# Performance work log

Hardware: AMD Instinct MI355X
Metric: run time of the kernel (lower is better)

The kernel has to match this reference:

```python
import jax, jax.numpy as jnp
import numpy as np

B = 1_048_576
W = 64  # hidden width
N_FREQ = 6   # 3 dims * 6 freqs * (sin,cos) = 36
K_BLOB = 4   # one-blob bins per dim


def _freq_embed(p):
    # [B,3] -> [B,36]
    freqs = 2.0 ** jnp.arange(N_FREQ, dtype=p.dtype)
    ang = jnp.pi * p[:, :, None] * freqs  # [B,3,6]
    return jnp.concatenate([jnp.sin(ang), jnp.cos(ang)], axis=-1).reshape(p.shape[0], 3 * 2 * N_FREQ)


def _sph(d):
    # unit-square parameterization of a direction, [B,3] -> [B,2]
    d = d / (jnp.linalg.norm(d, axis=-1, keepdims=True) + 1e-8)
    u = jnp.arctan2(d[:, 1], d[:, 0]) / (2.0 * jnp.pi) + 0.5
    v = jnp.arccos(jnp.clip(d[:, 2], -1.0 + 1e-6, 1.0 - 1e-6)) / jnp.pi
    return jnp.stack([u, v], axis=-1)


def _one_blob(x, k=K_BLOB):
    # x in [0,1], [B,D] -> [B,D*k] Gaussian one-blob encoding
    centers = (jnp.arange(k, dtype=x.dtype) + 0.5) / k
    sigma = 1.0 / k
    g = jnp.exp(-0.5 * ((x[..., None] - centers) / sigma) ** 2)  # [B,D,k]
    return g.reshape(x.shape[0], -1)


def _encode(p, wi, n, alpha, beta, r):
    ones = jnp.ones((p.shape[0], 2), dtype=p.dtype)
    return jnp.concatenate([
        _freq_embed(p),                      # 36
        _one_blob(_sph(wi)),                 # 8
        _one_blob(_sph(n)),                  # 8
        _one_blob(1.0 - jnp.exp(-r)),        # 4
        alpha, beta,                         # 6
        ones,                                # 2 (implicit bias)
    ], axis=-1)                              # -> [B,64]


def _mlp(x, Ws):
    h = x
    for Wk in Ws[:-1]:
        h = jax.nn.relu(h @ Wk.T)
    return h @ Ws[-1].T  # [B,3]


def setup_inputs() -> dict:
    key = jax.random.key(0)
    ks = jax.random.split(key, 13)
    p = jax.random.normal(ks[0], (B, 3), jnp.float32)
    wi = jax.random.normal(ks[1], (B, 3), jnp.float32)
    n = jax.random.normal(ks[2], (B, 3), jnp.float32)
    alpha = jax.random.uniform(ks[3], (B, 3), jnp.float32)
    beta = jax.random.uniform(ks[4], (B, 3), jnp.float32)
    r = jax.random.uniform(ks[5], (B, 1), jnp.float32)
    s = 1.0 / np.sqrt(W)
    weights = {}
    for i in range(6):
        weights[f"W{i}"] = jax.random.normal(ks[6 + i], (W, W), jnp.float32) * s
    weights["W6"] = jax.random.normal(ks[12], (3, W), jnp.float32) * s
    return dict(p=p, wi=wi, n=n, alpha=alpha, beta=beta, r=r, **weights)


def reference(p, wi, n, alpha, beta, r, W0, W1, W2, W3, W4, W5, W6):
    x = _encode(p, wi, n, alpha, beta, r)
    out = _mlp(x, [W0, W1, W2, W3, W4, W5, W6])
    return out * (alpha + beta)  # reflectance factorization
```

## Files before the change

### kernel.cpp

```cpp
#include <hip/hip_runtime.h>


typedef _Float16 f16;
typedef f16 f16x2 __attribute__((ext_vector_type(2)));
typedef f16 f16x4 __attribute__((ext_vector_type(4)));
typedef f16 f16x8 __attribute__((ext_vector_type(8)));
typedef float f32x4 __attribute__((ext_vector_type(4)));

#define MFMA32(A, B, C) __builtin_amdgcn_mfma_f32_16x16x32_f16(A, B, C, 0, 0, 0)

static constexpr int TILES  = 4;
static constexpr int WAVES  = 8;
static constexpr int BLOCK  = WAVES * 64;
static constexpr int PAIRS  = 4;
static constexpr int ROUNDS = 8;
static constexpr int SPB    = ROUNDS * PAIRS * 64;

static constexpr int    WUNITS   = 50;
static constexpr int    WCHUNKS  = WUNITS * 64;
static constexpr size_t WS_BYTES = (size_t)WCHUNKS * 16;
static constexpr int    LDSUNITS = 42;
static constexpr int    LDSCHNK  = LDSUNITS * 64;
static constexpr int    LDS_WEI  = LDSUNITS * 1024;
static constexpr int    LDS_STG  = PAIRS * 8192;
static constexpr int    LDS_TOT  = LDS_WEI + LDS_STG;

__host__ __device__ __forceinline__ int tau(int x) {
    return (x & 32) + ((x & 7) >> 2) * 16 + ((x >> 3) & 3) * 4 + (x & 3);
}

__device__ __forceinline__ f16x2 pkh(float a, float b) {
    return __builtin_bit_cast(f16x2, __builtin_amdgcn_cvt_pkrtz(a, b));
}

__device__ __forceinline__ f16x4 cat22(f16x2 a, f16x2 b) {
    return __builtin_shufflevector(a, b, 0, 1, 2, 3);
}

__device__ __forceinline__ f16x8 cat44(f16x4 a, f16x4 b) {
    return __builtin_shufflevector(a, b, 0, 1, 2, 3, 4, 5, 6, 7);
}

__device__ __forceinline__ f16x4 pack4(f32x4 v) {
    return cat22(pkh(v[0], v[1]), pkh(v[2], v[3]));
}

__device__ __forceinline__ float fast_atan2_rev(float y, float x) {
    const float ax = __builtin_fabsf(x), ay = __builtin_fabsf(y);
    const float mx = fmaxf(ax, ay), mn = fminf(ax, ay);
    const float a = mn * __builtin_amdgcn_rcpf(fmaxf(mx, 1e-30f));
    const float s = a * a;
    float r = a * (0.99997726f + s * (-0.33262347f + s * (0.19354346f +
              s * (-0.11643287f + s * (0.05265332f - s * 0.01172120f)))));
    if (ay > ax) r = 1.5707963268f - r;
    if (x < 0.0f) r = 3.1415926536f - r;
    r = (y < 0.0f) ? -r : r;
    return r * 0.15915494309189535f;
}

__device__ __forceinline__ float fast_acos(float x) {
    const float ax = __builtin_fabsf(x);
    const float t = __builtin_amdgcn_sqrtf(1.0f - ax);
    const float p = t * (1.5707288f + ax * (-0.2121144f +
                    ax * (0.0742610f - ax * 0.0187293f)));
    return (x < 0.0f) ? (3.1415926536f - p) : p;
}

__device__ __forceinline__ void blob4(float x, float* out) {
    const float dx = x - 0.125f;
    const float E0 = __expf(-8.0f * dx * dx);
    const float R  = __expf(4.0f * dx);
    const float t1 = R * 0.60653066f;
    const float t2 = R * 0.22313016f;
    const float t3 = R * 0.082084999f;
    out[0] = E0;
    out[1] = E0 * t1;
    out[2] = out[1] * t2;
    out[3] = out[2] * t3;
}

__device__ __forceinline__ f16x8 make_wchunk(
    int c, const float* __restrict__ W0, const float* __restrict__ W1,
    const float* __restrict__ W2, const float* __restrict__ W3,
    const float* __restrict__ W4, const float* __restrict__ W5,
    const float* __restrict__ W6)
{
    const int lane2 = c & 63;
    const int unit  = c >> 6;
    const int q = lane2 >> 4, m = lane2 & 15;
    f16x8 v;
    if (unit < 48) {
        const int l = unit >> 3, kt = (unit & 7) >> 2, mt = unit & 3;
        const float* Ws[6] = {W0, W1, W2, W3, W4, W5};
        const float* __restrict__ Wl = Ws[l];
#pragma unroll
        for (int j = 0; j < 8; ++j) {
            const int x = kt * 32 + q * 8 + j;
            const int src = (l == 0) ? x : tau(x);
            v[j] = (f16)Wl[(mt * 16 + m) * 64 + src];
        }
    } else {
        const int kt = unit - 48;
#pragma unroll
        for (int j = 0; j < 8; ++j) {
            const int src = tau(kt * 32 + q * 8 + j);
            v[j] = (m < 3) ? (f16)W6[m * 64 + src] : (f16)0.0f;
        }
    }
    return v;
}

__global__ __launch_bounds__(256, 1) void pack_weights_kernel(
    const float* __restrict__ W0, const float* __restrict__ W1,
    const float* __restrict__ W2, const float* __restrict__ W3,
    const float* __restrict__ W4, const float* __restrict__ W5,
    const float* __restrict__ W6, f16* __restrict__ ws)
{
    const int c = (int)blockIdx.x * 256 + threadIdx.x;
    if (c >= WCHUNKS) return;
    *(f16x8*)(ws + (size_t)c * 8) = make_wchunk(c, W0, W1, W2, W3, W4, W5, W6);
}

__device__ __forceinline__ void async_ld16(const void* g, void* l) {
    __builtin_amdgcn_global_load_lds(
        (const __attribute__((address_space(1))) void*)g,
        (__attribute__((address_space(3))) void*)l,
        16, 0, 0);
}

template<int PACKED>
__global__ __launch_bounds__(BLOCK, 4) void nrc_mlp_kernel(
    const float* __restrict__ P,  const float* __restrict__ WI,
    const float* __restrict__ NV, const float* __restrict__ AL,
    const float* __restrict__ BE, const float* __restrict__ RR,
    const f16*   __restrict__ ws,
    const float* __restrict__ W0, const float* __restrict__ W1,
    const float* __restrict__ W2, const float* __restrict__ W3,
    const float* __restrict__ W4, const float* __restrict__ W5,
    const float* __restrict__ W6, float* __restrict__ Out)
{
    __shared__ __attribute__((aligned(16))) unsigned char smem[LDS_TOT];

    const int tid  = threadIdx.x;
    const int lane = tid & 63;
    const int w    = tid >> 6;
    const int q    = lane >> 4;
    const int m    = lane & 15;
    const bool prod = (w < PAIRS);
    const int  p    = prod ? w : (w - PAIRS);
    const int  blk_base = (int)blockIdx.x * SPB;

    unsigned char* const stgp = smem + LDS_WEI + p * 8192;
    unsigned char* const wbl  = smem + lane * 16;

    if (PACKED) {
#pragma unroll
        for (int i = 0; i < 6; ++i) {
            const int c = i * BLOCK + tid;
            if (c < LDSCHNK)
                async_ld16(ws + (size_t)(512 + c) * 8, smem + c * 16);
        }
    } else {
#pragma unroll
        for (int i = 0; i < 6; ++i) {
            const int c = i * BLOCK + tid;
            if (c < LDSCHNK)
                *(f16x8*)(smem + c * 16) =
                    make_wchunk(512 + c, W0, W1, W2, W3, W4, W5, W6);
        }
    }

    const f16x4 zero4 = {(f16)0.0f, (f16)0.0f, (f16)0.0f, (f16)0.0f};
    const f32x4 ZF = {0.0f, 0.0f, 0.0f, 0.0f};

    f16x8 bf[TILES][2];

    auto compute = [&](int rr) {
        __builtin_amdgcn_s_setprio(1);
        f32x4 acc[TILES][4];
#pragma unroll
        for (int layer = 0; layer < 6; ++layer) {
            f16x8 wa[4];
            if (layer == 0) {
                if (PACKED) {
#pragma unroll
                    for (int mt = 0; mt < 4; ++mt)
                        wa[mt] = *(const f16x8*)(ws + (size_t)(mt * 64 + lane) * 8);
                } else {
#pragma unroll
                    for (int mt = 0; mt < 4; ++mt)
                        wa[mt] = make_wchunk(mt * 64 + lane, W0, W1, W2, W3, W4, W5, W6);
                }
            } else {
#pragma unroll
                for (int mt = 0; mt < 4; ++mt)
                    wa[mt] = *(const f16x8*)(wbl + ((layer - 1) * 8 + mt) * 1024);
            }
#pragma unroll
            for (int t = 0; t < TILES; ++t)
#pragma unroll
                for (int mt = 0; mt < 4; ++mt)
                    acc[t][mt] = MFMA32(wa[mt], bf[t][0], ZF);
            if (layer == 0) {
                if (PACKED) {
#pragma unroll
                    for (int mt = 0; mt < 4; ++mt)
                        wa[mt] = *(const f16x8*)(ws + (size_t)((4 + mt) * 64 + lane) * 8);
                } else {
#pragma unroll
                    for (int mt = 0; mt < 4; ++mt)
                        wa[mt] = make_wchunk((4 + mt) * 64 + lane, W0, W1, W2, W3, W4, W5, W6);
                }
            } else {
#pragma unroll
                for (int mt = 0; mt < 4; ++mt)
                    wa[mt] = *(const f16x8*)(wbl + ((layer - 1) * 8 + 4 + mt) * 1024);
            }
#pragma unroll
            for (int t = 0; t < TILES; ++t)
#pragma unroll
                for (int mt = 0; mt < 4; ++mt)
                    acc[t][mt] = MFMA32(wa[mt], bf[t][1], acc[t][mt]);
#pragma unroll
            for (int t = 0; t < TILES; ++t) {
                f16x4 pk[4];
#pragma unroll
                for (int mt = 0; mt < 4; ++mt)
                    pk[mt] = __builtin_elementwise_max(pack4(acc[t][mt]), zero4);
                bf[t][0] = cat44(pk[0], pk[1]);
                bf[t][1] = cat44(pk[2], pk[3]);
            }
        }
        __builtin_amdgcn_s_setprio(0);
        const int rbase = blk_base + rr * (PAIRS * 64) + p * 64;
        float aa[TILES][3];
#pragma unroll
        for (int t = 0; t < TILES; ++t) {
            const int s = rbase + t * 16 + m;
#pragma unroll
            for (int d = 0; d < 3; ++d)
                aa[t][d] = AL[s * 3 + d] + BE[s * 3 + d];
        }
        f32x4 oz[TILES];
        {
            const f16x8 w6a = *(const f16x8*)(wbl + 40 * 1024);
#pragma unroll
            for (int t = 0; t < TILES; ++t) oz[t] = MFMA32(w6a, bf[t][0], ZF);
            const f16x8 w6b = *(const f16x8*)(wbl + 41 * 1024);
#pragma unroll
            for (int t = 0; t < TILES; ++t) oz[t] = MFMA32(w6b, bf[t][1], oz[t]);
        }
#pragma unroll
        for (int t = 0; t < TILES; ++t) {
            if (lane < 16) {
                const int s = rbase + t * 16 + m;
                float* o = Out + s * 3;
                o[0] = oz[t][0] * aa[t][0];
                o[1] = oz[t][1] * aa[t][1];
                o[2] = oz[t][2] * aa[t][2];
            }
        }
    };

    for (int r = 0; r < ROUNDS; ++r) {
        if (prod) {
#pragma unroll
            for (int t = 0; t < TILES; ++t) {
                bf[t][0] = f16x8{};
                bf[t][1] = f16x8{};
            }
            const int s = blk_base + r * (PAIRS * 64) + p * 64 + lane;
            unsigned char* const myrow = stgp + lane * 128;
            const int rot = (lane * 4) & 31;
            auto put = [&](int D, f16x2 a, f16x2 b) {
                *(f16x4*)(myrow + (((D + rot) & 31) << 2)) = cat22(a, b);
            };

            const float3 pv = *(const float3*)(P  + 3 * s);
            const float3 wv = *(const float3*)(WI + 3 * s);
            const float3 nv = *(const float3*)(NV + 3 * s);
            const float3 av = *(const float3*)(AL + 3 * s);
            const float3 bv = *(const float3*)(BE + 3 * s);
            const float  rv = RR[s];
            const float parr[3] = {pv.x, pv.y, pv.z};

#pragma unroll
            for (int d = 0; d < 3; ++d) {
                float sA[6], cA[6];
                const float fr = __builtin_amdgcn_fractf(parr[d] * 0.5f);
                sA[0] = __builtin_amdgcn_sinf(fr);
                cA[0] = __builtin_amdgcn_cosf(fr);
#pragma unroll
                for (int k = 1; k < 6; ++k) {
                    const float s2 = sA[k-1] * sA[k-1];
                    const float sc = sA[k-1] * cA[k-1];
                    cA[k] = fmaf(-2.0f, s2, 1.0f);
                    sA[k] = sc + sc;
                }
                put(6 * d + 0, pkh(sA[0], sA[1]), pkh(sA[2], sA[3]));
                put(6 * d + 2, pkh(sA[4], sA[5]), pkh(cA[0], cA[1]));
                put(6 * d + 4, pkh(cA[2], cA[3]), pkh(cA[4], cA[5]));
            }
#pragma unroll
            for (int which = 0; which < 2; ++which) {
                const float3 dv3 = (which == 0) ? wv : nv;
                const float dx = dv3.x, dy = dv3.y, dz = dv3.z;
                const int D0 = 18 + which * 4;
                const float nr = __builtin_amdgcn_sqrtf(dx*dx + dy*dy + dz*dz) + 1e-8f;
                const float u  = fast_atan2_rev(dy, dx) + 0.5f;
                float zc = dz * __builtin_amdgcn_rcpf(nr);
                zc = fminf(fmaxf(zc, -1.0f + 1e-6f), 1.0f - 1e-6f);
                const float vv = fast_acos(zc) * 0.3183098861837907f;
                float ob[8];
                blob4(u,  &ob[0]);
                blob4(vv, &ob[4]);
                put(D0,     pkh(ob[0], ob[1]), pkh(ob[2], ob[3]));
                put(D0 + 2, pkh(ob[4], ob[5]), pkh(ob[6], ob[7]));
            }
            {
                float ob[4];
                blob4(1.0f - __expf(-rv), ob);
                put(26, pkh(ob[0], ob[1]), pkh(ob[2], ob[3]));
            }
            put(28, pkh(av.x, av.y), pkh(av.z, bv.x));
            put(30, pkh(bv.y, bv.z), pkh(1.0f, 1.0f));
        } else if (r > 0) {
            compute(r - 1);
        }

        __syncthreads();

        if (!prod) {
#pragma unroll
            for (int t = 0; t < TILES; ++t) {
                const int n = t * 16 + m;
#pragma unroll
                for (int kt = 0; kt < 2; ++kt) {
                    const int s0 = (16 * kt + 4 * q + 4 * m) & 31;
                    bf[t][kt] = *(const f16x8*)(stgp + n * 128 + (s0 << 2));
                }
            }
        }

        __syncthreads();
    }
    if (!prod) compute(ROUNDS - 1);
}

extern "C" void kernel_launch(void* const* d_in, const int* in_sizes, int n_in,
                              void* d_out, int out_size, void* d_ws, size_t ws_size,
                              hipStream_t stream) {
    (void)n_in; (void)out_size;
    const float* P  = (const float*)d_in[0];
    const float* WI = (const float*)d_in[1];
    const float* NV = (const float*)d_in[2];
    const float* AL = (const float*)d_in[3];
    const float* BE = (const float*)d_in[4];
    const float* RR = (const float*)d_in[5];
    const float* W0 = (const float*)d_in[6];
    const float* W1 = (const float*)d_in[7];
    const float* W2 = (const float*)d_in[8];
    const float* W3 = (const float*)d_in[9];
    const float* W4 = (const float*)d_in[10];
    const float* W5 = (const float*)d_in[11];
    const float* W6 = (const float*)d_in[12];
    f16*   ws  = (f16*)d_ws;
    float* Out = (float*)d_out;

    const int Bn = in_sizes[0] / 3;
    const int grid = Bn / SPB;

    if (ws_size >= WS_BYTES) {
        hipLaunchKernelGGL(pack_weights_kernel, dim3((WCHUNKS + 255) / 256),
                           dim3(256), 0, stream, W0, W1, W2, W3, W4, W5, W6, ws);
        hipLaunchKernelGGL((nrc_mlp_kernel<1>), dim3(grid), dim3(BLOCK), 0, stream,
                           P, WI, NV, AL, BE, RR, ws,
                           W0, W1, W2, W3, W4, W5, W6, Out);
    } else {
        hipLaunchKernelGGL((nrc_mlp_kernel<0>), dim3(grid), dim3(BLOCK), 0, stream,
                           P, WI, NV, AL, BE, RR, ws,
                           W0, W1, W2, W3, W4, W5, W6, Out);
    }
}
```

Measured before the change: 173.8 us.

## Replace producer/consumer wave split with per-wave software-pipelined encode+MLP

After: 160.3 us. 7.8% less time.

```diff
diff --git a/kernel.cpp b/kernel.cpp
--- a/kernel.cpp
+++ b/kernel.cpp
@@ -8,13 +8,13 @@
 typedef float f32x4 __attribute__((ext_vector_type(4)));
 
 #define MFMA32(A, B, C) __builtin_amdgcn_mfma_f32_16x16x32_f16(A, B, C, 0, 0, 0)
+#define LDS_FENCE() __asm__ volatile("" ::: "memory")
 
 static constexpr int TILES  = 4;
-static constexpr int WAVES  = 8;
+static constexpr int WAVES  = 4;
 static constexpr int BLOCK  = WAVES * 64;
-static constexpr int PAIRS  = 4;
-static constexpr int ROUNDS = 8;
-static constexpr int SPB    = ROUNDS * PAIRS * 64;
+static constexpr int NB     = 8;
+static constexpr int SPB    = WAVES * NB * 64;
 
 static constexpr int    WUNITS   = 50;
 static constexpr int    WCHUNKS  = WUNITS * 64;
@@ -22,7 +22,7 @@
 static constexpr int    LDSUNITS = 42;
 static constexpr int    LDSCHNK  = LDSUNITS * 64;
 static constexpr int    LDS_WEI  = LDSUNITS * 1024;
-static constexpr int    LDS_STG  = PAIRS * 8192;
+static constexpr int    LDS_STG  = WAVES * 8192;
 static constexpr int    LDS_TOT  = LDS_WEI + LDS_STG;
 
 __host__ __device__ __forceinline__ int tau(int x) {
@@ -128,8 +128,80 @@
         16, 0, 0);
 }
 
+struct EncIn {
+    float pv[3], wv[3], nv[3], av[3], bv[3], rv;
+};
+
+__device__ __forceinline__ EncIn load_inputs(
+    const float* __restrict__ P,  const float* __restrict__ WI,
+    const float* __restrict__ NV, const float* __restrict__ AL,
+    const float* __restrict__ BE, const float* __restrict__ RR, int s)
+{
+    EncIn e;
+#pragma unroll
+    for (int d = 0; d < 3; ++d) {
+        e.pv[d] = P [s * 3 + d];
+        e.wv[d] = WI[s * 3 + d];
+        e.nv[d] = NV[s * 3 + d];
+        e.av[d] = AL[s * 3 + d];
+        e.bv[d] = BE[s * 3 + d];
+    }
+    e.rv = RR[s];
+    return e;
+}
+
+__device__ __forceinline__ void enc_slice(
+    int k, const EncIn& e, unsigned char* myrow, int rot, float* abn)
+{
+    auto put = [&](int D, f16x2 a, f16x2 b) {
+        *(f16x4*)(myrow + (((D + rot) & 31) << 2)) = cat22(a, b);
+    };
+    if (k <= 2) {
+        const int d = k;
+        float sA[6], cA[6];
+        const float fr = __builtin_amdgcn_fractf(e.pv[d] * 0.5f);
+        sA[0] = __builtin_amdgcn_sinf(fr);
+        cA[0] = __builtin_amdgcn_cosf(fr);
+#pragma unroll
+        for (int kk = 1; kk < 6; ++kk) {
+            const float s2 = sA[kk-1] * sA[kk-1];
+            const float sc = sA[kk-1] * cA[kk-1];
+            cA[kk] = fmaf(-2.0f, s2, 1.0f);
+            sA[kk] = sc + sc;
+        }
+        put(6*d + 0, pkh(sA[0], sA[1]), pkh(sA[2], sA[3]));
+        put(6*d + 2, pkh(sA[4], sA[5]), pkh(cA[0], cA[1]));
+        put(6*d + 4, pkh(cA[2], cA[3]), pkh(cA[4], cA[5]));
+    } else if (k <= 4) {
+        const int which = k - 3;
+        const float dx = which ? e.nv[0] : e.wv[0];
+        const float dy = which ? e.nv[1] : e.wv[1];
+        const float dz = which ? e.nv[2] : e.wv[2];
+        const int D0 = 18 + which * 4;
+        const float nr = __builtin_amdgcn_sqrtf(dx*dx + dy*dy + dz*dz) + 1e-8f;
+        const float u  = fast_atan2_rev(dy, dx) + 0.5f;
+        float zc = dz * __builtin_amdgcn_rcpf(nr);
+        zc = fminf(fmaxf(zc, -1.0f + 1e-6f), 1.0f - 1e-6f);
+        const float vv = fast_acos(zc) * 0.3183098861837907f;
+        float ob[8];
+        blob4(u,  &ob[0]);
+        blob4(vv, &ob[4]);
+        put(D0,     pkh(ob[0], ob[1]), pkh(ob[2], ob[3]));
+        put(D0 + 2, pkh(ob[4], ob[5]), pkh(ob[6], ob[7]));
+    } else {
+        float ob[4];
+        blob4(1.0f - __expf(-e.rv), ob);
+        put(26, pkh(ob[0], ob[1]), pkh(ob[2], ob[3]));
+        put(28, pkh(e.av[0], e.av[1]), pkh(e.av[2], e.bv[0]));
+        put(30, pkh(e.bv[1], e.bv[2]), pkh(1.0f, 1.0f));
+        abn[0] = e.av[0] + e.bv[0];
+        abn[1] = e.av[1] + e.bv[1];
+        abn[2] = e.av[2] + e.bv[2];
+    }
+}
+
 template<int PACKED>
-__global__ __launch_bounds__(BLOCK, 4) void nrc_mlp_kernel(
+__global__ __launch_bounds__(BLOCK, 2) void nrc_mlp_kernel(
     const float* __restrict__ P,  const float* __restrict__ WI,
     const float* __restrict__ NV, const float* __restrict__ AL,
     const float* __restrict__ BE, const float* __restrict__ RR,
@@ -146,23 +218,23 @@
     const int w    = tid >> 6;
     const int q    = lane >> 4;
     const int m    = lane & 15;
-    const bool prod = (w < PAIRS);
-    const int  p    = prod ? w : (w - PAIRS);
-    const int  blk_base = (int)blockIdx.x * SPB;
-
-    unsigned char* const stgp = smem + LDS_WEI + p * 8192;
-    unsigned char* const wbl  = smem + lane * 16;
+    const int wave_base = (int)blockIdx.x * SPB + w * (NB * 64);
+
+    unsigned char* const stgw  = smem + LDS_WEI + w * 8192;
+    unsigned char* const myrow = stgw + lane * 128;
+    const int rot = (lane * 4) & 31;
+    unsigned char* const wbl   = smem + lane * 16;
 
     if (PACKED) {
 #pragma unroll
-        for (int i = 0; i < 6; ++i) {
+        for (int i = 0; i < (LDSCHNK + BLOCK - 1) / BLOCK; ++i) {
             const int c = i * BLOCK + tid;
             if (c < LDSCHNK)
                 async_ld16(ws + (size_t)(512 + c) * 8, smem + c * 16);
         }
     } else {
 #pragma unroll
-        for (int i = 0; i < 6; ++i) {
+        for (int i = 0; i < (LDSCHNK + BLOCK - 1) / BLOCK; ++i) {
             const int c = i * BLOCK + tid;
             if (c < LDSCHNK)
                 *(f16x8*)(smem + c * 16) =
@@ -170,27 +242,60 @@
         }
     }
 
+    f16x8 w0f[8];
+    if (PACKED) {
+#pragma unroll
+        for (int f = 0; f < 8; ++f)
+            w0f[f] = *(const f16x8*)(ws + (size_t)(f * 64 + lane) * 8);
+    } else {
+#pragma unroll
+        for (int f = 0; f < 8; ++f)
+            w0f[f] = make_wchunk(f * 64 + lane, W0, W1, W2, W3, W4, W5, W6);
+    }
+
+    float ab_cur[3], abn[3];
+    {
+        EncIn e0 = load_inputs(P, WI, NV, AL, BE, RR, wave_base + lane);
+#pragma unroll
+        for (int k = 0; k < 6; ++k)
+            enc_slice(k, e0, myrow, rot, abn);
+        ab_cur[0] = abn[0]; ab_cur[1] = abn[1]; ab_cur[2] = abn[2];
+    }
+
+    __syncthreads();
+
     const f16x4 zero4 = {(f16)0.0f, (f16)0.0f, (f16)0.0f, (f16)0.0f};
     const f32x4 ZF = {0.0f, 0.0f, 0.0f, 0.0f};
 
     f16x8 bf[TILES][2];
-
-    auto compute = [&](int rr) {
-        __builtin_amdgcn_s_setprio(1);
+    LDS_FENCE();
+#pragma unroll
+    for (int t = 0; t < TILES; ++t)
+#pragma unroll
+        for (int kt = 0; kt < 2; ++kt) {
+            const int s0 = (16 * kt + 4 * q + 4 * m) & 31;
+            bf[t][kt] = *(const f16x8*)(stgw + (t * 16 + m) * 128 + (s0 << 2));
+        }
+    LDS_FENCE();
+
+    EncIn cur = load_inputs(P, WI, NV, AL, BE, RR, wave_base + 64 + lane);
+    EncIn nxt = cur;
+
+#pragma unroll 1
+    for (int b = 0; b < NB; ++b) {
+        const bool hn = (b + 1 < NB);
+        if (b + 2 < NB)
+            nxt = load_inputs(P, WI, NV, AL, BE, RR,
+                              wave_base + (b + 2) * 64 + lane);
+
         f32x4 acc[TILES][4];
 #pragma unroll
         for (int layer = 0; layer < 6; ++layer) {
             f16x8 wa[4];
+            __builtin_amdgcn_s_setprio(1);
             if (layer == 0) {
-                if (PACKED) {
-#pragma unroll
-                    for (int mt = 0; mt < 4; ++mt)
-                        wa[mt] = *(const f16x8*)(ws + (size_t)(mt * 64 + lane) * 8);
-                } else {
-#pragma unroll
-                    for (int mt = 0; mt < 4; ++mt)
-                        wa[mt] = make_wchunk(mt * 64 + lane, W0, W1, W2, W3, W4, W5, W6);
-                }
+#pragma unroll
+                for (int mt = 0; mt < 4; ++mt) wa[mt] = w0f[mt];
             } else {
 #pragma unroll
                 for (int mt = 0; mt < 4; ++mt)
@@ -202,15 +307,8 @@
                 for (int mt = 0; mt < 4; ++mt)
                     acc[t][mt] = MFMA32(wa[mt], bf[t][0], ZF);
             if (layer == 0) {
-                if (PACKED) {
-#pragma unroll
-                    for (int mt = 0; mt < 4; ++mt)
-                        wa[mt] = *(const f16x8*)(ws + (size_t)((4 + mt) * 64 + lane) * 8);
-                } else {
-#pragma unroll
-                    for (int mt = 0; mt < 4; ++mt)
-                        wa[mt] = make_wchunk((4 + mt) * 64 + lane, W0, W1, W2, W3, W4, W5, W6);
-                }
+#pragma unroll
+                for (int mt = 0; mt < 4; ++mt) wa[mt] = w0f[4 + mt];
             } else {
 #pragma unroll
                 for (int mt = 0; mt < 4; ++mt)
@@ -221,6 +319,10 @@
 #pragma unroll
                 for (int mt = 0; mt < 4; ++mt)
                     acc[t][mt] = MFMA32(wa[mt], bf[t][1], acc[t][mt]);
+            __builtin_amdgcn_s_setprio(0);
+
+            if (hn) enc_slice(layer, cur, myrow, rot, abn);
+
 #pragma unroll
             for (int t = 0; t < TILES; ++t) {
                 f16x4 pk[4];
@@ -231,120 +333,46 @@
                 bf[t][1] = cat44(pk[2], pk[3]);
             }
         }
-        __builtin_amdgcn_s_setprio(0);
-        const int rbase = blk_base + rr * (PAIRS * 64) + p * 64;
-        float aa[TILES][3];
-#pragma unroll
-        for (int t = 0; t < TILES; ++t) {
-            const int s = rbase + t * 16 + m;
-#pragma unroll
-            for (int d = 0; d < 3; ++d)
-                aa[t][d] = AL[s * 3 + d] + BE[s * 3 + d];
-        }
-        f32x4 oz[TILES];
+
         {
+            const int rbase = wave_base + b * 64;
+            f32x4 oz[TILES];
             const f16x8 w6a = *(const f16x8*)(wbl + 40 * 1024);
 #pragma unroll
             for (int t = 0; t < TILES; ++t) oz[t] = MFMA32(w6a, bf[t][0], ZF);
             const f16x8 w6b = *(const f16x8*)(wbl + 41 * 1024);
 #pragma unroll
             for (int t = 0; t < TILES; ++t) oz[t] = MFMA32(w6b, bf[t][1], oz[t]);
-        }
-#pragma unroll
-        for (int t = 0; t < TILES; ++t) {
-            if (lane < 16) {
-                const int s = rbase + t * 16 + m;
-                float* o = Out + s * 3;
-                o[0] = oz[t][0] * aa[t][0];
-                o[1] = oz[t][1] * aa[t][1];
-                o[2] = oz[t][2] * aa[t][2];
+#pragma unroll
+            for (int t = 0; t < TILES; ++t) {
+                const float s0 = __shfl(ab_cur[0], t * 16 + m);
+                const float s1 = __shfl(ab_cur[1], t * 16 + m);
+                const float s2 = __shfl(ab_cur[2], t * 16 + m);
+                if (lane < 16) {
+                    const int s = rbase + t * 16 + m;
+                    float* o = Out + s * 3;
+                    o[0] = oz[t][0] * s0;
+                    o[1] = oz[t][1] * s1;
+                    o[2] = oz[t][2] * s2;
+                }
             }
         }
-    };
-
-    for (int r = 0; r < ROUNDS; ++r) {
-        if (prod) {
-#pragma unroll
-            for (int t = 0; t < TILES; ++t) {
-                bf[t][0] = f16x8{};
-                bf[t][1] = f16x8{};
-            }
-            const int s = blk_base + r * (PAIRS * 64) + p * 64 + lane;
-            unsigned char* const myrow = stgp + lane * 128;
-            const int rot = (lane * 4) & 31;
-            auto put = [&](int D, f16x2 a, f16x2 b) {
-                *(f16x4*)(myrow + (((D + rot) & 31) << 2)) = cat22(a, b);
-            };
-
-            const float3 pv = *(const float3*)(P  + 3 * s);
-            const float3 wv = *(const float3*)(WI + 3 * s);
-            const float3 nv = *(const float3*)(NV + 3 * s);
-            const float3 av = *(const float3*)(AL + 3 * s);
-            const float3 bv = *(const float3*)(BE + 3 * s);
-            const float  rv = RR[s];
-            const float parr[3] = {pv.x, pv.y, pv.z};
-
-#pragma unroll
-            for (int d = 0; d < 3; ++d) {
-                float sA[6], cA[6];
-                const float fr = __builtin_amdgcn_fractf(parr[d] * 0.5f);
-                sA[0] = __builtin_amdgcn_sinf(fr);
-                cA[0] = __builtin_amdgcn_cosf(fr);
-#pragma unroll
-                for (int k = 1; k < 6; ++k) {
-                    const float s2 = sA[k-1] * sA[k-1];
-                    const float sc = sA[k-1] * cA[k-1];
-                    cA[k] = fmaf(-2.0f, s2, 1.0f);
-                    sA[k] = sc + sc;
-                }
-                put(6 * d + 0, pkh(sA[0], sA[1]), pkh(sA[2], sA[3]));
-                put(6 * d + 2, pkh(sA[4], sA[5]), pkh(cA[0], cA[1]));
-                put(6 * d + 4, pkh(cA[2], cA[3]), pkh(cA[4], cA[5]));
-            }
-#pragma unroll
-            for (int which = 0; which < 2; ++which) {
-                const float3 dv3 = (which == 0) ? wv : nv;
-                const float dx = dv3.x, dy = dv3.y, dz = dv3.z;
-                const int D0 = 18 + which * 4;
-                const float nr = __builtin_amdgcn_sqrtf(dx*dx + dy*dy + dz*dz) + 1e-8f;
-                const float u  = fast_atan2_rev(dy, dx) + 0.5f;
-                float zc = dz * __builtin_amdgcn_rcpf(nr);
-                zc = fminf(fmaxf(zc, -1.0f + 1e-6f), 1.0f - 1e-6f);
-                const float vv = fast_acos(zc) * 0.3183098861837907f;
-                float ob[8];
-                blob4(u,  &ob[0]);
-                blob4(vv, &ob[4]);
-                put(D0,     pkh(ob[0], ob[1]), pkh(ob[2], ob[3]));
-                put(D0 + 2, pkh(ob[4], ob[5]), pkh(ob[6], ob[7]));
-            }
-            {
-                float ob[4];
-                blob4(1.0f - __expf(-rv), ob);
-                put(26, pkh(ob[0], ob[1]), pkh(ob[2], ob[3]));
-            }
-            put(28, pkh(av.x, av.y), pkh(av.z, bv.x));
-            put(30, pkh(bv.y, bv.z), pkh(1.0f, 1.0f));
-        } else if (r > 0) {
-            compute(r - 1);
-        }
-
-        __syncthreads();
-
-        if (!prod) {
-#pragma unroll
-            for (int t = 0; t < TILES; ++t) {
-                const int n = t * 16 + m;
+
+        if (hn) {
+            ab_cur[0] = abn[0]; ab_cur[1] = abn[1]; ab_cur[2] = abn[2];
+            LDS_FENCE();
+#pragma unroll
+            for (int t = 0; t < TILES; ++t)
 #pragma unroll
                 for (int kt = 0; kt < 2; ++kt) {
                     const int s0 = (16 * kt + 4 * q + 4 * m) & 31;
-                    bf[t][kt] = *(const f16x8*)(stgp + n * 128 + (s0 << 2));
+                    bf[t][kt] = *(const f16x8*)(
+                        stgw + (t * 16 + m) * 128 + (s0 << 2));
                 }
-            }
-        }
-
-        __syncthreads();
-    }
-    if (!prod) compute(ROUNDS - 1);
+            LDS_FENCE();
+            cur = nxt;
+        }
+    }
 }
 
 extern "C" void kernel_launch(void* const* d_in, const int* in_sizes, int n_in,
```
